# Optimization experiments

Hardware: AMD Instinct MI355X
Metric: run time of the kernel (lower is better)

## Reference

```python
import jax, jax.numpy as jnp
import numpy as np

NEG_SLOPE = 0.2
EPS = 1e-16

N_NODES = 50000
N_EDGES = 800000
IN_DIM = 64
HEADS = 4
HEAD_DIM = 64


def setup_inputs() -> dict:
    key = jax.random.key(0)
    k1, k2, k3, k4, k5 = jax.random.split(key, 5)
    x = jax.random.normal(k1, (N_NODES, IN_DIM), dtype=jnp.float32)
    edge_index = jax.random.randint(k2, (2, N_EDGES), 0, N_NODES, dtype=jnp.int64)
    W = jax.random.normal(k3, (IN_DIM, HEADS * HEAD_DIM), dtype=jnp.float32) * (1.0 / np.sqrt(IN_DIM))
    att_src = jax.random.normal(k4, (HEADS, HEAD_DIM), dtype=jnp.float32) * 0.1
    att_dst = jax.random.normal(k5, (HEADS, HEAD_DIM), dtype=jnp.float32) * 0.1
    bias = jnp.zeros((HEADS * HEAD_DIM,), dtype=jnp.float32)
    return {"x": x, "edge_index": edge_index, "W": W,
            "att_src": att_src, "att_dst": att_dst, "bias": bias}


def reference(x, edge_index, W, att_src, att_dst, bias):
    N = x.shape[0]
    H, D = att_src.shape
    # add self-loops (PyG default add_self_loops=True)
    loop = jnp.arange(N, dtype=edge_index.dtype)
    src = jnp.concatenate([edge_index[0], loop])  # message source j
    dst = jnp.concatenate([edge_index[1], loop])  # message target i

    h = (x @ W).reshape(N, H, D)                 # [N,H,D] per-head projection
    a_src = jnp.einsum('nhd,hd->nh', h, att_src)  # [N,H]
    a_dst = jnp.einsum('nhd,hd->nh', h, att_dst)  # [N,H]

    score = jax.nn.leaky_relu(a_src[src] + a_dst[dst], NEG_SLOPE)  # [E,H]
    # segment softmax over edges grouped by destination node
    m = jax.ops.segment_max(score, dst, num_segments=N)            # [N,H]
    m = jnp.where(jnp.isfinite(m), m, 0.0)
    e = jnp.exp(score - m[dst])                                    # [E,H]
    denom = jax.ops.segment_sum(e, dst, num_segments=N)            # [N,H]
    alpha = e / (denom[dst] + EPS)                                 # [E,H]

    msgs = h[src] * alpha[:, :, None]                              # [E,H,D]
    out = jax.ops.segment_sum(msgs, dst, num_segments=N)           # [N,H,D]
    return out.reshape(N, H * D) + bias
```

## Files before the change

### kernel.cpp

```cpp
#include <hip/hip_runtime.h>

#define N_NODES 50000
#define N_EDGES 800000
#define E_TOT   850000
#define HD      256
#define MAXDEG  64
#define NEG_SLOPE 0.2f
#define EPS 1e-16f

typedef __attribute__((ext_vector_type(8))) short short8;
typedef __attribute__((ext_vector_type(4))) float f32x4;

__device__ __forceinline__ unsigned short f2bf(float f) {
    union { float f; unsigned int i; } c; c.f = f;
    unsigned int r = 0x7fffu + ((c.i >> 16) & 1u);
    return (unsigned short)((c.i + r) >> 16);
}
__device__ __forceinline__ short8 pack8(float4 a, float4 b) {
    short8 r;
    r[0] = (short)f2bf(a.x); r[1] = (short)f2bf(a.y);
    r[2] = (short)f2bf(a.z); r[3] = (short)f2bf(a.w);
    r[4] = (short)f2bf(b.x); r[5] = (short)f2bf(b.y);
    r[6] = (short)f2bf(b.z); r[7] = (short)f2bf(b.w);
    return r;
}
__device__ __forceinline__ float lrelu_exp(float v) {
    v = (v < 0.f) ? v * NEG_SLOPE : v;
    return __expf(v);
}

__global__ __launch_bounds__(256) void prep_kernel(
        const float* __restrict__ W, const float* __restrict__ att_src,
        const float* __restrict__ att_dst, float* __restrict__ ws, float* __restrict__ wd) {
    const int t = threadIdx.x, head = t >> 6, k = t & 63;
    const float* wrow = W + k * 256 + head * 64;
    const float* as = att_src + head * 64;
    const float* adv = att_dst + head * 64;
    float s = 0.f, d = 0.f;
#pragma unroll 8
    for (int j = 0; j < 64; ++j) { s += wrow[j] * as[j]; d += wrow[j] * adv[j]; }
    ws[k * 4 + head] = s;
    wd[k * 4 + head] = d;
}

__global__ __launch_bounds__(256) void logit_bucket_kernel(
        const float* __restrict__ x,
        const float4* __restrict__ ws4, const float4* __restrict__ wd4,
        const int* __restrict__ eidx, int* __restrict__ cnt, int* __restrict__ slot,
        float4* __restrict__ a_src4, float4* __restrict__ a_dst4) {
    const int g = blockIdx.x * 256 + threadIdx.x;
    if (g < E_TOT) {
        int s, d;
        if (g < N_EDGES) { s = eidx[g]; d = eidx[N_EDGES + g]; }
        else             { s = d = g - N_EDGES; }
        int pos = atomicAdd(&cnt[d], 1);
        if (pos < MAXDEG) slot[d * MAXDEG + pos] = s;
    }

    if (g < N_NODES) {
        const float4* xr = (const float4*)(x + (size_t)g * 64);
        float4 vs = {0.f, 0.f, 0.f, 0.f};
        float4 vd = {0.f, 0.f, 0.f, 0.f};
#pragma unroll 4
        for (int kk = 0; kk < 16; ++kk) {
            float4 xv = xr[kk];
#pragma unroll
            for (int j = 0; j < 4; ++j) {
                const float xj = j == 0 ? xv.x : j == 1 ? xv.y : j == 2 ? xv.z : xv.w;
                const float4 w1 = ws4[kk * 4 + j];
                const float4 w2 = wd4[kk * 4 + j];
                vs.x += xj * w1.x; vs.y += xj * w1.y; vs.z += xj * w1.z; vs.w += xj * w1.w;
                vd.x += xj * w2.x; vd.y += xj * w2.y; vd.z += xj * w2.z; vd.w += xj * w2.w;
            }
        }
        a_src4[g] = vs;
        a_dst4[g] = vd;
    }
}

__global__ __launch_bounds__(256) void aggregate_x_kernel(
        const int* __restrict__ cnt, const int* __restrict__ slot,
        const float4* __restrict__ a_src4, const float4* __restrict__ a_dst4,
        const float* __restrict__ x, unsigned short* __restrict__ yb) {
    __shared__ int    lsrc[4][64];
    __shared__ float4 lscs[4][64];
    const int w    = threadIdx.x >> 6;
    const int lane = threadIdx.x & 63;
    const int node = blockIdx.x * 4 + w;
    int deg = cnt[node];
    if (deg > MAXDEG) deg = MAXDEG;
    const int base = node * MAXDEG;
    const float4 ad = a_dst4[node];

    int s = (lane < deg) ? slot[base + lane] : 0;
    float4 A = a_src4[s];
    float4 sc;
    if (lane < deg) {
        sc.x = lrelu_exp(A.x + ad.x); sc.y = lrelu_exp(A.y + ad.y);
        sc.z = lrelu_exp(A.z + ad.z); sc.w = lrelu_exp(A.w + ad.w);
    } else {
        sc = (float4){0.f, 0.f, 0.f, 0.f};
    }
    lsrc[w][lane] = s;
    lscs[w][lane] = sc;

    float4 ds = sc;
#pragma unroll
    for (int m = 1; m < 64; m <<= 1) {
        ds.x += __shfl_xor(ds.x, m, 64); ds.y += __shfl_xor(ds.y, m, 64);
        ds.z += __shfl_xor(ds.z, m, 64); ds.w += __shfl_xor(ds.w, m, 64);
    }
    float4 inv;
    inv.x = 1.f / (ds.x + EPS); inv.y = 1.f / (ds.y + EPS);
    inv.z = 1.f / (ds.z + EPS); inv.w = 1.f / (ds.w + EPS);

    float4 acc = {0.f, 0.f, 0.f, 0.f};
    int e = 0;
    for (; e + 3 < deg; e += 4) {
        int s0 = lsrc[w][e + 0], s1 = lsrc[w][e + 1];
        int s2 = lsrc[w][e + 2], s3 = lsrc[w][e + 3];
        float4 c0 = lscs[w][e + 0], c1 = lscs[w][e + 1];
        float4 c2 = lscs[w][e + 2], c3 = lscs[w][e + 3];
        float x0 = x[(size_t)s0 * 64 + lane];
        float x1 = x[(size_t)s1 * 64 + lane];
        float x2 = x[(size_t)s2 * 64 + lane];
        float x3 = x[(size_t)s3 * 64 + lane];
        acc.x += x0 * c0.x + x1 * c1.x + x2 * c2.x + x3 * c3.x;
        acc.y += x0 * c0.y + x1 * c1.y + x2 * c2.y + x3 * c3.y;
        acc.z += x0 * c0.z + x1 * c1.z + x2 * c2.z + x3 * c3.z;
        acc.w += x0 * c0.w + x1 * c1.w + x2 * c2.w + x3 * c3.w;
    }
    for (; e < deg; ++e) {
        int se = lsrc[w][e];
        float4 ce = lscs[w][e];
        float xv = x[(size_t)se * 64 + lane];
        acc.x += xv * ce.x; acc.y += xv * ce.y;
        acc.z += xv * ce.z; acc.w += xv * ce.w;
    }
    unsigned short* yp = yb + (size_t)node * 256 + lane;
    yp[  0] = f2bf(acc.x * inv.x);
    yp[ 64] = f2bf(acc.y * inv.y);
    yp[128] = f2bf(acc.z * inv.z);
    yp[192] = f2bf(acc.w * inv.w);
}

__global__ __launch_bounds__(256) void gemm_out_kernel(
        const unsigned short* __restrict__ yb, const float* __restrict__ W,
        const float* __restrict__ bias, float* __restrict__ out) {
    __shared__ __align__(16) unsigned short Wt[256 * 64];
    const int t = threadIdx.x;
    {
        const int c = t;
        for (int kg = 0; kg < 8; ++kg) {
            float4 lo, hi;
            lo.x = W[(kg * 8 + 0) * 256 + c]; lo.y = W[(kg * 8 + 1) * 256 + c];
            lo.z = W[(kg * 8 + 2) * 256 + c]; lo.w = W[(kg * 8 + 3) * 256 + c];
            hi.x = W[(kg * 8 + 4) * 256 + c]; hi.y = W[(kg * 8 + 5) * 256 + c];
            hi.z = W[(kg * 8 + 6) * 256 + c]; hi.w = W[(kg * 8 + 7) * 256 + c];
            *(short8*)&Wt[c * 64 + ((kg ^ (c & 7)) << 3)] = pack8(lo, hi);
        }
    }
    __syncthreads();

    const int wave = t >> 6, lane = t & 63;
    const int q = lane >> 4, mloc = lane & 15;
    const int rowbase = blockIdx.x * 64 + wave * 16;
    int arow = rowbase + mloc;
    if (arow > N_NODES - 1) arow = N_NODES - 1;

    short8 a0[4], a1[4];
#pragma unroll
    for (int h = 0; h < 4; ++h) {
        const unsigned short* yr = yb + (size_t)arow * 256 + h * 64;
        a0[h] = *(const short8*)&yr[q * 8];
        a1[h] = *(const short8*)&yr[32 + q * 8];
    }

    f32x4 acc[16];
#pragma unroll
    for (int n = 0; n < 16; ++n) acc[n] = (f32x4){0.f, 0.f, 0.f, 0.f};
#pragma unroll
    for (int n = 0; n < 16; ++n) {
        const int c = n * 16 + mloc;
        const int h = n >> 2;
        const unsigned short* rowp = &Wt[c * 64];
        short8 b0 = *(const short8*)&rowp[((q    ) ^ (c & 7)) << 3];
        short8 b1 = *(const short8*)&rowp[((4 + q) ^ (c & 7)) << 3];
        acc[n] = __builtin_amdgcn_mfma_f32_16x16x32_bf16(a0[h], b0, acc[n], 0, 0, 0);
        acc[n] = __builtin_amdgcn_mfma_f32_16x16x32_bf16(a1[h], b1, acc[n], 0, 0, 0);
    }

    float bv[16];
#pragma unroll
    for (int n = 0; n < 16; ++n) bv[n] = bias[n * 16 + mloc];

    const int orow = rowbase + q * 4;
#pragma unroll
    for (int r = 0; r < 4; ++r) {
        if (orow + r < N_NODES) {
            float* op = out + (size_t)(orow + r) * 256 + mloc;
#pragma unroll
            for (int n = 0; n < 16; ++n) op[n * 16] = acc[n][r] + bv[n];
        }
    }
}

extern "C" void kernel_launch(void* const* d_in, const int* in_sizes, int n_in,
                              void* d_out, int out_size, void* d_ws, size_t ws_size,
                              hipStream_t stream) {
    const float* x       = (const float*)d_in[0];
    const int*   eidx    = (const int*)  d_in[1];
    const float* W       = (const float*)d_in[2];
    const float* att_src = (const float*)d_in[3];
    const float* att_dst = (const float*)d_in[4];
    const float* bias    = (const float*)d_in[5];
    float* out = (float*)d_out;

    unsigned short* yb = (unsigned short*)d_ws;
    float* a_src = (float*)(yb + (size_t)N_NODES * HD);
    float* a_dst = a_src + N_NODES * 4;
    float* ws    = a_dst + N_NODES * 4;
    float* wd    = ws + 256;
    int*   cnt   = (int*)(wd + 256);
    int*   slot  = cnt + N_NODES;

    hipMemsetAsync(cnt, 0, N_NODES * sizeof(int), stream);
    prep_kernel<<<1, 256, 0, stream>>>(W, att_src, att_dst, ws, wd);
    logit_bucket_kernel<<<(E_TOT + 255) / 256, 256, 0, stream>>>(
        x, (const float4*)ws, (const float4*)wd, eidx, cnt, slot,
        (float4*)a_src, (float4*)a_dst);
    aggregate_x_kernel<<<N_NODES / 4, 256, 0, stream>>>(
        cnt, slot, (const float4*)a_src, (const float4*)a_dst, x, yb);
    gemm_out_kernel<<<(N_NODES + 63) / 64, 256, 0, stream>>>(yb, W, bias, out);
}
```

Before: 181.7 us.

## Fuse aggregation with output GEMM, convert x to bf16, shrink slot indices

Merges the neighbour aggregation and the MFMA output GEMM into one kernel that stages aggregated rows in LDS, so the bf16 intermediate never goes to global memory. Precomputes a bf16 copy of x and a swizzled bf16 W in global memory inside a combined prep kernel, so gathers move half the bytes and blocks no longer rebuild W in LDS. Stores slot indices as 16-bit values, which truncates node ids above 65535; that holds only for N=50000. It also spreads the per-node logit computation across threads (one thread per 17), and the fused kernel has only 782 blocks of 4 waves, each processing 16 nodes serially, so latency hiding may suffer.

```diff
diff --git a/kernel.cpp b/kernel.cpp
--- a/kernel.cpp
+++ b/kernel.cpp
@@ -3,7 +3,6 @@
 #define N_NODES 50000
 #define N_EDGES 800000
 #define E_TOT   850000
-#define HD      256
 #define MAXDEG  64
 #define NEG_SLOPE 0.2f
 #define EPS 1e-16f
@@ -15,6 +14,10 @@
     union { float f; unsigned int i; } c; c.f = f;
     unsigned int r = 0x7fffu + ((c.i >> 16) & 1u);
     return (unsigned short)((c.i + r) >> 16);
+}
+__device__ __forceinline__ float bf2f(unsigned short u) {
+    union { unsigned int i; float f; } c; c.i = ((unsigned int)u) << 16;
+    return c.f;
 }
 __device__ __forceinline__ short8 pack8(float4 a, float4 b) {
     short8 r;
@@ -29,24 +32,46 @@
     return __expf(v);
 }
 
-__global__ __launch_bounds__(256) void prep_kernel(
-        const float* __restrict__ W, const float* __restrict__ att_src,
-        const float* __restrict__ att_dst, float* __restrict__ ws, float* __restrict__ wd) {
-    const int t = threadIdx.x, head = t >> 6, k = t & 63;
-    const float* wrow = W + k * 256 + head * 64;
-    const float* as = att_src + head * 64;
-    const float* adv = att_dst + head * 64;
-    float s = 0.f, d = 0.f;
+__global__ __launch_bounds__(256) void prep_all_kernel(
+        const float4* __restrict__ x4, const float* __restrict__ W,
+        const float* __restrict__ att_src, const float* __restrict__ att_dst,
+        ushort4* __restrict__ xb4, float* __restrict__ ws, float* __restrict__ wd,
+        unsigned short* __restrict__ Wtbf) {
+    const int b = blockIdx.x, t = threadIdx.x;
+    if (b < 3125) {
+        const int i = b * 256 + t;
+        float4 v = x4[i];
+        ushort4 u;
+        u.x = f2bf(v.x); u.y = f2bf(v.y); u.z = f2bf(v.z); u.w = f2bf(v.w);
+        xb4[i] = u;
+    } else if (b == 3125) {
+        const int head = t >> 6, k = t & 63;
+        const float* wrow = W + k * 256 + head * 64;
+        const float* as = att_src + head * 64;
+        const float* adv = att_dst + head * 64;
+        float s = 0.f, d = 0.f;
 #pragma unroll 8
-    for (int j = 0; j < 64; ++j) { s += wrow[j] * as[j]; d += wrow[j] * adv[j]; }
-    ws[k * 4 + head] = s;
-    wd[k * 4 + head] = d;
+        for (int j = 0; j < 64; ++j) { s += wrow[j] * as[j]; d += wrow[j] * adv[j]; }
+        ws[k * 4 + head] = s;
+        wd[k * 4 + head] = d;
+    } else {
+        const int c = t;
+        for (int kg = 0; kg < 8; ++kg) {
+            float4 lo, hi;
+            lo.x = W[(kg * 8 + 0) * 256 + c]; lo.y = W[(kg * 8 + 1) * 256 + c];
+            lo.z = W[(kg * 8 + 2) * 256 + c]; lo.w = W[(kg * 8 + 3) * 256 + c];
+            hi.x = W[(kg * 8 + 4) * 256 + c]; hi.y = W[(kg * 8 + 5) * 256 + c];
+            hi.z = W[(kg * 8 + 6) * 256 + c]; hi.w = W[(kg * 8 + 7) * 256 + c];
+            *(short8*)&Wtbf[c * 64 + ((kg ^ (c & 7)) << 3)] = pack8(lo, hi);
+        }
+    }
 }
 
 __global__ __launch_bounds__(256) void logit_bucket_kernel(
         const float* __restrict__ x,
         const float4* __restrict__ ws4, const float4* __restrict__ wd4,
-        const int* __restrict__ eidx, int* __restrict__ cnt, int* __restrict__ slot,
+        const int* __restrict__ eidx, int* __restrict__ cnt,
+        unsigned short* __restrict__ slotb,
         float4* __restrict__ a_src4, float4* __restrict__ a_dst4) {
     const int g = blockIdx.x * 256 + threadIdx.x;
     if (g < E_TOT) {
@@ -54,11 +79,12 @@
         if (g < N_EDGES) { s = eidx[g]; d = eidx[N_EDGES + g]; }
         else             { s = d = g - N_EDGES; }
         int pos = atomicAdd(&cnt[d], 1);
-        if (pos < MAXDEG) slot[d * MAXDEG + pos] = s;
-    }
-
-    if (g < N_NODES) {
-        const float4* xr = (const float4*)(x + (size_t)g * 64);
+        if (pos < MAXDEG) slotb[d * MAXDEG + pos] = (unsigned short)s;
+    }
+
+    const int node = g / 17;
+    if (g - node * 17 == 0 && node < N_NODES) {
+        const float4* xr = (const float4*)(x + (size_t)node * 64);
         float4 vs = {0.f, 0.f, 0.f, 0.f};
         float4 vd = {0.f, 0.f, 0.f, 0.f};
 #pragma unroll 4
@@ -73,107 +99,90 @@
                 vd.x += xj * w2.x; vd.y += xj * w2.y; vd.z += xj * w2.z; vd.w += xj * w2.w;
             }
         }
-        a_src4[g] = vs;
-        a_dst4[g] = vd;
-    }
-}
-
-__global__ __launch_bounds__(256) void aggregate_x_kernel(
-        const int* __restrict__ cnt, const int* __restrict__ slot,
+        a_src4[node] = vs;
+        a_dst4[node] = vd;
+    }
+}
+
+__global__ __launch_bounds__(256) void aggregate_gemm_kernel(
+        const int* __restrict__ cnt, const unsigned short* __restrict__ slotb,
         const float4* __restrict__ a_src4, const float4* __restrict__ a_dst4,
-        const float* __restrict__ x, unsigned short* __restrict__ yb) {
+        const unsigned short* __restrict__ xb, const unsigned short* __restrict__ Wtbf,
+        const float* __restrict__ bias, float* __restrict__ out) {
     __shared__ int    lsrc[4][64];
     __shared__ float4 lscs[4][64];
+    __shared__ __align__(16) unsigned short ylds[64 * 256];
     const int w    = threadIdx.x >> 6;
     const int lane = threadIdx.x & 63;
-    const int node = blockIdx.x * 4 + w;
-    int deg = cnt[node];
-    if (deg > MAXDEG) deg = MAXDEG;
-    const int base = node * MAXDEG;
-    const float4 ad = a_dst4[node];
-
-    int s = (lane < deg) ? slot[base + lane] : 0;
-    float4 A = a_src4[s];
-    float4 sc;
-    if (lane < deg) {
-        sc.x = lrelu_exp(A.x + ad.x); sc.y = lrelu_exp(A.y + ad.y);
-        sc.z = lrelu_exp(A.z + ad.z); sc.w = lrelu_exp(A.w + ad.w);
-    } else {
-        sc = (float4){0.f, 0.f, 0.f, 0.f};
-    }
-    lsrc[w][lane] = s;
-    lscs[w][lane] = sc;
-
-    float4 ds = sc;
-#pragma unroll
-    for (int m = 1; m < 64; m <<= 1) {
-        ds.x += __shfl_xor(ds.x, m, 64); ds.y += __shfl_xor(ds.y, m, 64);
-        ds.z += __shfl_xor(ds.z, m, 64); ds.w += __shfl_xor(ds.w, m, 64);
-    }
-    float4 inv;
-    inv.x = 1.f / (ds.x + EPS); inv.y = 1.f / (ds.y + EPS);
-    inv.z = 1.f / (ds.z + EPS); inv.w = 1.f / (ds.w + EPS);
-
-    float4 acc = {0.f, 0.f, 0.f, 0.f};
-    int e = 0;
-    for (; e + 3 < deg; e += 4) {
-        int s0 = lsrc[w][e + 0], s1 = lsrc[w][e + 1];
-        int s2 = lsrc[w][e + 2], s3 = lsrc[w][e + 3];
-        float4 c0 = lscs[w][e + 0], c1 = lscs[w][e + 1];
-        float4 c2 = lscs[w][e + 2], c3 = lscs[w][e + 3];
-        float x0 = x[(size_t)s0 * 64 + lane];
-        float x1 = x[(size_t)s1 * 64 + lane];
-        float x2 = x[(size_t)s2 * 64 + lane];
-        float x3 = x[(size_t)s3 * 64 + lane];
-        acc.x += x0 * c0.x + x1 * c1.x + x2 * c2.x + x3 * c3.x;
-        acc.y += x0 * c0.y + x1 * c1.y + x2 * c2.y + x3 * c3.y;
-        acc.z += x0 * c0.z + x1 * c1.z + x2 * c2.z + x3 * c3.z;
-        acc.w += x0 * c0.w + x1 * c1.w + x2 * c2.w + x3 * c3.w;
-    }
-    for (; e < deg; ++e) {
-        int se = lsrc[w][e];
-        float4 ce = lscs[w][e];
-        float xv = x[(size_t)se * 64 + lane];
-        acc.x += xv * ce.x; acc.y += xv * ce.y;
-        acc.z += xv * ce.z; acc.w += xv * ce.w;
-    }
-    unsigned short* yp = yb + (size_t)node * 256 + lane;
-    yp[  0] = f2bf(acc.x * inv.x);
-    yp[ 64] = f2bf(acc.y * inv.y);
-    yp[128] = f2bf(acc.z * inv.z);
-    yp[192] = f2bf(acc.w * inv.w);
-}
-
-__global__ __launch_bounds__(256) void gemm_out_kernel(
-        const unsigned short* __restrict__ yb, const float* __restrict__ W,
-        const float* __restrict__ bias, float* __restrict__ out) {
-    __shared__ __align__(16) unsigned short Wt[256 * 64];
-    const int t = threadIdx.x;
-    {
-        const int c = t;
-        for (int kg = 0; kg < 8; ++kg) {
-            float4 lo, hi;
-            lo.x = W[(kg * 8 + 0) * 256 + c]; lo.y = W[(kg * 8 + 1) * 256 + c];
-            lo.z = W[(kg * 8 + 2) * 256 + c]; lo.w = W[(kg * 8 + 3) * 256 + c];
-            hi.x = W[(kg * 8 + 4) * 256 + c]; hi.y = W[(kg * 8 + 5) * 256 + c];
-            hi.z = W[(kg * 8 + 6) * 256 + c]; hi.w = W[(kg * 8 + 7) * 256 + c];
-            *(short8*)&Wt[c * 64 + ((kg ^ (c & 7)) << 3)] = pack8(lo, hi);
-        }
-    }
-    __syncthreads();
-
-    const int wave = t >> 6, lane = t & 63;
+    const int rowbase = blockIdx.x * 64 + w * 16;
+
+    for (int i = 0; i < 16; ++i) {
+        const int node = rowbase + i;
+        const int m = w * 16 + i;
+        float4 acc = {0.f, 0.f, 0.f, 0.f};
+        float4 inv = {0.f, 0.f, 0.f, 0.f};
+        if (node < N_NODES) {
+            int deg = cnt[node];
+            if (deg > MAXDEG) deg = MAXDEG;
+            const float4 ad = a_dst4[node];
+            int s = (lane < deg) ? (int)slotb[node * MAXDEG + lane] : 0;
+            float4 A = a_src4[s];
+            float4 sc = {0.f, 0.f, 0.f, 0.f};
+            if (lane < deg) {
+                sc.x = lrelu_exp(A.x + ad.x); sc.y = lrelu_exp(A.y + ad.y);
+                sc.z = lrelu_exp(A.z + ad.z); sc.w = lrelu_exp(A.w + ad.w);
+            }
+            lsrc[w][lane] = s;
+            lscs[w][lane] = sc;
+            float4 dv = sc;
+#pragma unroll
+            for (int mm = 1; mm < 64; mm <<= 1) {
+                dv.x += __shfl_xor(dv.x, mm, 64); dv.y += __shfl_xor(dv.y, mm, 64);
+                dv.z += __shfl_xor(dv.z, mm, 64); dv.w += __shfl_xor(dv.w, mm, 64);
+            }
+            inv.x = 1.f / (dv.x + EPS); inv.y = 1.f / (dv.y + EPS);
+            inv.z = 1.f / (dv.z + EPS); inv.w = 1.f / (dv.w + EPS);
+
+            int e = 0;
+            for (; e + 3 < deg; e += 4) {
+                int s0 = lsrc[w][e + 0], s1 = lsrc[w][e + 1];
+                int s2 = lsrc[w][e + 2], s3 = lsrc[w][e + 3];
+                float4 c0 = lscs[w][e + 0], c1 = lscs[w][e + 1];
+                float4 c2 = lscs[w][e + 2], c3 = lscs[w][e + 3];
+                float x0 = bf2f(xb[(size_t)s0 * 64 + lane]);
+                float x1 = bf2f(xb[(size_t)s1 * 64 + lane]);
+                float x2 = bf2f(xb[(size_t)s2 * 64 + lane]);
+                float x3 = bf2f(xb[(size_t)s3 * 64 + lane]);
+                acc.x += x0 * c0.x + x1 * c1.x + x2 * c2.x + x3 * c3.x;
+                acc.y += x0 * c0.y + x1 * c1.y + x2 * c2.y + x3 * c3.y;
+                acc.z += x0 * c0.z + x1 * c1.z + x2 * c2.z + x3 * c3.z;
+                acc.w += x0 * c0.w + x1 * c1.w + x2 * c2.w + x3 * c3.w;
+            }
+            for (; e < deg; ++e) {
+                int se = lsrc[w][e];
+                float4 ce = lscs[w][e];
+                float xv = bf2f(xb[(size_t)se * 64 + lane]);
+                acc.x += xv * ce.x; acc.y += xv * ce.y;
+                acc.z += xv * ce.z; acc.w += xv * ce.w;
+            }
+        }
+        const int lhi = lane >> 3, llo = lane & 7;
+#pragma unroll
+        for (int h = 0; h < 4; ++h) {
+            const float yv = h == 0 ? acc.x * inv.x : h == 1 ? acc.y * inv.y
+                           : h == 2 ? acc.z * inv.z : acc.w * inv.w;
+            ylds[m * 256 + (((h * 8 + lhi) ^ (m & 7)) << 3) + llo] = f2bf(yv);
+        }
+    }
+
     const int q = lane >> 4, mloc = lane & 15;
-    const int rowbase = blockIdx.x * 64 + wave * 16;
-    int arow = rowbase + mloc;
-    if (arow > N_NODES - 1) arow = N_NODES - 1;
+    const int m = w * 16 + mloc;
 
     short8 a0[4], a1[4];
 #pragma unroll
     for (int h = 0; h < 4; ++h) {
-        const unsigned short* yr = yb + (size_t)arow * 256 + h * 64;
-        a0[h] = *(const short8*)&yr[q * 8];
-        a1[h] = *(const short8*)&yr[32 + q * 8];
+        a0[h] = *(const short8*)&ylds[m * 256 + (((h * 8 + q    ) ^ (m & 7)) << 3)];
+        a1[h] = *(const short8*)&ylds[m * 256 + (((h * 8 + 4 + q) ^ (m & 7)) << 3)];
     }
 
     f32x4 acc[16];
@@ -183,7 +192,7 @@
     for (int n = 0; n < 16; ++n) {
         const int c = n * 16 + mloc;
         const int h = n >> 2;
-        const unsigned short* rowp = &Wt[c * 64];
+        const unsigned short* rowp = Wtbf + c * 64;
         short8 b0 = *(const short8*)&rowp[((q    ) ^ (c & 7)) << 3];
         short8 b1 = *(const short8*)&rowp[((4 + q) ^ (c & 7)) << 3];
         acc[n] = __builtin_amdgcn_mfma_f32_16x16x32_bf16(a0[h], b0, acc[n], 0, 0, 0);
@@ -194,7 +203,7 @@
 #pragma unroll
     for (int n = 0; n < 16; ++n) bv[n] = bias[n * 16 + mloc];
 
-    const int orow = rowbase + q * 4;
+    const int orow = blockIdx.x * 64 + w * 16 + q * 4;
 #pragma unroll
     for (int r = 0; r < 4; ++r) {
         if (orow + r < N_NODES) {
@@ -216,20 +225,22 @@
     const float* bias    = (const float*)d_in[5];
     float* out = (float*)d_out;
 
-    unsigned short* yb = (unsigned short*)d_ws;
-    float* a_src = (float*)(yb + (size_t)N_NODES * HD);
+    float* fws   = (float*)d_ws;
+    float* a_src = fws;
     float* a_dst = a_src + N_NODES * 4;
-    float* ws    = a_dst + N_NODES * 4;
-    float* wd    = ws + 256;
-    int*   cnt   = (int*)(wd + 256);
-    int*   slot  = cnt + N_NODES;
+    float* wsv   = a_dst + N_NODES * 4;
+    float* wdv   = wsv + 256;
+    int*   cnt   = (int*)(wdv + 256);
+    unsigned short* xb    = (unsigned short*)(cnt + N_NODES);
+    unsigned short* Wtbf  = xb + (size_t)N_NODES * 64;
+    unsigned short* slotb = Wtbf + 256 * 64;
 
     hipMemsetAsync(cnt, 0, N_NODES * sizeof(int), stream);
-    prep_kernel<<<1, 256, 0, stream>>>(W, att_src, att_dst, ws, wd);
+    prep_all_kernel<<<3127, 256, 0, stream>>>(
+        (const float4*)x, W, att_src, att_dst, (ushort4*)xb, wsv, wdv, Wtbf);
     logit_bucket_kernel<<<(E_TOT + 255) / 256, 256, 0, stream>>>(
-        x, (const float4*)ws, (const float4*)wd, eidx, cnt, slot,
+        x, (const float4*)wsv, (const float4*)wdv, eidx, cnt, slotb,
         (float4*)a_src, (float4*)a_dst);
-    aggregate_x_kernel<<<N_NODES / 4, 256, 0, stream>>>(
-        cnt, slot, (const float4*)a_src, (const float4*)a_dst, x, yb);
-    gemm_out_kernel<<<(N_NODES + 63) / 64, 256, 0, stream>>>(yb, W, bias, out);
-}
+    aggregate_gemm_kernel<<<(N_NODES + 63) / 64, 256, 0, stream>>>(
+        cnt, slotb, (const float4*)a_src, (const float4*)a_dst, xb, Wtbf, bias, out);
+}
```

New measurement: 206.4 us. 1.14x slower.
